# Optimization experiments

Hardware: AMD Instinct MI355X
Metric: run time of the kernel (lower is better)

Reference implementation:

```python
import jax, jax.numpy as jnp
import numpy as np

RO = 0.5      # backtracking shrink factor (default ro)
C = 1e-4      # Armijo constant (default c)


def setup_inputs() -> dict:
    B, TX = 65536, 8
    n = 2 * TX
    key = jax.random.key(0)
    k1, k2, k3 = jax.random.split(key, 3)
    y = jax.random.normal(k1, (B, n), dtype=jnp.float32)
    h = jax.random.normal(k2, (B, n, n), dtype=jnp.float32)
    bits = jax.random.randint(k3, (B, n, 1), 0, 2)
    x0 = (2 * bits - 1).astype(jnp.float32)  # random +/-1 init (torch.randint path)
    return {"y": y, "h": h, "x0": x0, "iteration": 10}


def reference(y, h, x0, iteration):
    B, n = y.shape
    y3 = y[..., None]                      # [B, n, 1]
    hT = jnp.swapaxes(h, 1, 2)             # [B, n, n]
    h_k = jnp.tile(jnp.eye(n, dtype=y.dtype)[None], (B, 1, 1))
    x = x0
    alpha = jnp.ones((B,), dtype=y.dtype)  # NOTE: alpha persists across outer iters, as in torch

    def f_val(xc):                         # torch.norm(y - h x, dim=1) / 2 -> [B, 1]
        r = y3 - h @ xc
        return 0.5 * jnp.sqrt(jnp.sum(r * r, axis=1))

    def g_val(xc):                         # H^T (H x - y) -> [B, n, 1]
        return hT @ (h @ xc - y3)

    for _ in range(iteration):
        g = g_val(x)
        p = -(h_k @ g)                     # search direction [B, n, 1]

        # --- backtracking line search (Armijo), batched; cond is any() over batch ---
        fx = f_val(x)[:, 0]                                    # [B]
        gtp = (jnp.swapaxes(g, 1, 2) @ p)[:, 0, 0]             # [B]

        def _lhs(a):
            return f_val(x + a[:, None, None] * p)[:, 0]

        def cond_fn(a):
            return jnp.any(_lhs(a) > fx + C * a * gtp)

        def body_fn(a):
            return jnp.where(_lhs(a) > fx + C * a * gtp, RO * a, a)

        alpha = jax.lax.while_loop(cond_fn, body_fn, alpha)

        # --- step + BFGS inverse-Hessian update (as written in the source) ---
        x_new = x + alpha[:, None, None] * p
        s = x_new - x                                          # [B, n, 1]
        yk = g_val(x_new) - g                                  # [B, n, 1]
        sT = jnp.swapaxes(s, 1, 2)
        ykT = jnp.swapaxes(yk, 1, 2)
        auxSc = sT @ yk                                        # [B, 1, 1]
        h_k = (h_k
               + (auxSc + ykT @ (h_k @ yk)) * (s @ sT) / auxSc ** 2
               - ((h_k @ (yk @ sT)) + s @ (ykT @ h_k)) / auxSc)
        x = x_new

    return x[..., 0]                       # [B, n]
```

## Files before the change

kernel.cpp:

```cpp
#include <hip/hip_runtime.h>


#define QN_N 16

__device__ __forceinline__ float redsum16(float v) {
    v += __shfl_xor(v, 1);
    v += __shfl_xor(v, 2);
    v += __shfl_xor(v, 4);
    v += __shfl_xor(v, 8);
    return v;
}

__device__ __forceinline__ float dot16(const float* a, const float* b) {
    float s0 = 0.f, s1 = 0.f, s2 = 0.f, s3 = 0.f;
#pragma unroll
    for (int k = 0; k < QN_N; k += 4) {
        s0 = fmaf(a[k + 0], b[k + 0], s0);
        s1 = fmaf(a[k + 1], b[k + 1], s1);
        s2 = fmaf(a[k + 2], b[k + 2], s2);
        s3 = fmaf(a[k + 3], b[k + 3], s3);
    }
    return (s0 + s1) + (s2 + s3);
}

#define BCAST(val, dst)                                   \
    do {                                                  \
        __builtin_amdgcn_wave_barrier();                  \
        slot[l] = (val);                                  \
        __builtin_amdgcn_wave_barrier();                  \
        float4 b0_ = ((const float4*)slot)[0];            \
        float4 b1_ = ((const float4*)slot)[1];            \
        float4 b2_ = ((const float4*)slot)[2];            \
        float4 b3_ = ((const float4*)slot)[3];            \
        (dst)[0] = b0_.x; (dst)[1] = b0_.y;               \
        (dst)[2] = b0_.z; (dst)[3] = b0_.w;               \
        (dst)[4] = b1_.x; (dst)[5] = b1_.y;               \
        (dst)[6] = b1_.z; (dst)[7] = b1_.w;               \
        (dst)[8] = b2_.x; (dst)[9] = b2_.y;               \
        (dst)[10] = b2_.z; (dst)[11] = b2_.w;             \
        (dst)[12] = b3_.x; (dst)[13] = b3_.y;             \
        (dst)[14] = b3_.z; (dst)[15] = b3_.w;             \
    } while (0)

__global__ __launch_bounds__(256, 4) void qn_kernel(
    const float* __restrict__ y, const float* __restrict__ h,
    const float* __restrict__ x0, const int* __restrict__ iter_p,
    float* __restrict__ out, int B)
{
    const int tid = blockIdx.x * blockDim.x + threadIdx.x;
    const int batch = tid >> 4;
    const int l = threadIdx.x & 15;
    if (batch >= B) return;
    const int iters = iter_p[0];

    __shared__ __align__(16) float bc[16][QN_N];
    float* slot = bc[threadIdx.x >> 4];

    const float* hb = h + (size_t)batch * (QN_N * QN_N);
    float hrow[QN_N], hcol[QN_N], hk[QN_N];
    {
        const float4* r4 = (const float4*)(hb + l * QN_N);
#pragma unroll
        for (int q = 0; q < 4; ++q) {
            float4 v = r4[q];
            hrow[4 * q + 0] = v.x; hrow[4 * q + 1] = v.y;
            hrow[4 * q + 2] = v.z; hrow[4 * q + 3] = v.w;
        }
    }
#pragma unroll
    for (int i = 0; i < QN_N; ++i) hcol[i] = hb[i * QN_N + l];
#pragma unroll
    for (int i = 0; i < QN_N; ++i) hk[i] = (i == l) ? 1.0f : 0.0f;

    const float yl = y[batch * QN_N + l];
    float xl = x0[batch * QN_N + l];
    float alpha = 1.0f;

    float tmp[QN_N];

    BCAST(xl, tmp);
    float hx = dot16(hrow, tmp);
    BCAST(hx - yl, tmp);
    float g = dot16(hcol, tmp);

    for (int it = 0; it < iters; ++it) {
        BCAST(g, tmp);
        float p = -dot16(hk, tmp);
        float gtp = redsum16(g * p);
        BCAST(p, tmp);
        float hp = dot16(hrow, tmp);
        float r0 = yl - hx;
        float fx = 0.5f * sqrtf(redsum16(r0 * r0));

        float a = alpha;
        float hxa;
        for (;;) {
            hxa = hx + a * hp;
            float res = yl - hxa;
            float lhs = 0.5f * sqrtf(redsum16(res * res));
            float rhs = fx + 1e-4f * a * gtp;
            bool fail = lhs > rhs;
            if (!__any(fail)) break;
            if (fail) a *= 0.5f;
        }
        alpha = a;

        float ap = a * p;
        float xn = xl + ap;
        float s = xn - xl;
        float hxn = hxa;

        BCAST(hxn - yl, tmp);
        float gn = dot16(hcol, tmp);
        float yk = gn - g;

        BCAST(yk, tmp);
        float hy = dot16(hk, tmp);

        float aux = redsum16(s * yk);
        float yhy = redsum16(yk * hy);
        float inv_aux = 1.0f / aux;
        float inv_aux2 = 1.0f / (aux * aux);
        float A1 = aux + yhy;

        float sv[QN_N], hyv[QN_N];
        BCAST(s, sv);
        BCAST(hy, hyv);
#pragma unroll
        for (int k = 0; k < QN_N; ++k) {
            float t1 = (A1 * (s * sv[k])) * inv_aux2;
            float t2 = (hy * sv[k] + s * hyv[k]) * inv_aux;
            hk[k] = (hk[k] + t1) - t2;
        }

        xl = xn;
        hx = hxn;
        g = gn;
    }

    out[batch * QN_N + l] = xl;
}

extern "C" void kernel_launch(void* const* d_in, const int* in_sizes, int n_in,
                              void* d_out, int out_size, void* d_ws, size_t ws_size,
                              hipStream_t stream) {
    const float* y  = (const float*)d_in[0];
    const float* h  = (const float*)d_in[1];
    const float* x0 = (const float*)d_in[2];
    const int* itp  = (const int*)d_in[3];
    float* out = (float*)d_out;

    const int B = in_sizes[0] / QN_N;
    const int threads = B * QN_N;
    const int blocks = (threads + 255) / 256;
    qn_kernel<<<blocks, 256, 0, stream>>>(y, h, x0, itp, out, B);
}
```

Before: 174.3 us.

## Use packed f32x2 FMAs, merge reductions and broadcasts, refactor BFGS update

Converts the per-lane 16-element dot products and the inverse-Hessian row update to two-wide float vectors so the compiler can emit packed FP32 FMA instructions. Pairs of independent 16-lane shuffle reductions and two shared-memory broadcasts are merged into single passes, and the shared slot is widened to hold both broadcast vectors. The BFGS update is refactored by precomputing the per-lane scalar coefficients, which changes floating-point rounding order slightly. The goal is fewer VALU instructions and fewer barrier/shuffle round trips per iteration.

```diff
diff --git a/kernel.cpp b/kernel.cpp
--- a/kernel.cpp
+++ b/kernel.cpp
@@ -2,6 +2,10 @@
 
 
 #define QN_N 16
+
+typedef float f32x2 __attribute__((ext_vector_type(2)));
+
+#define SLOT_STRIDE 40
 
 __device__ __forceinline__ float redsum16(float v) {
     v += __shfl_xor(v, 1);
@@ -11,35 +15,59 @@
     return v;
 }
 
-__device__ __forceinline__ float dot16(const float* a, const float* b) {
-    float s0 = 0.f, s1 = 0.f, s2 = 0.f, s3 = 0.f;
+__device__ __forceinline__ f32x2 redsum16p(f32x2 v) {
 #pragma unroll
-    for (int k = 0; k < QN_N; k += 4) {
-        s0 = fmaf(a[k + 0], b[k + 0], s0);
-        s1 = fmaf(a[k + 1], b[k + 1], s1);
-        s2 = fmaf(a[k + 2], b[k + 2], s2);
-        s3 = fmaf(a[k + 3], b[k + 3], s3);
+    for (int m = 1; m <= 8; m <<= 1) {
+        f32x2 o;
+        o.x = __shfl_xor(v.x, m);
+        o.y = __shfl_xor(v.y, m);
+        v = v + o;
     }
-    return (s0 + s1) + (s2 + s3);
+    return v;
 }
 
-#define BCAST(val, dst)                                   \
-    do {                                                  \
-        __builtin_amdgcn_wave_barrier();                  \
-        slot[l] = (val);                                  \
-        __builtin_amdgcn_wave_barrier();                  \
-        float4 b0_ = ((const float4*)slot)[0];            \
-        float4 b1_ = ((const float4*)slot)[1];            \
-        float4 b2_ = ((const float4*)slot)[2];            \
-        float4 b3_ = ((const float4*)slot)[3];            \
-        (dst)[0] = b0_.x; (dst)[1] = b0_.y;               \
-        (dst)[2] = b0_.z; (dst)[3] = b0_.w;               \
-        (dst)[4] = b1_.x; (dst)[5] = b1_.y;               \
-        (dst)[6] = b1_.z; (dst)[7] = b1_.w;               \
-        (dst)[8] = b2_.x; (dst)[9] = b2_.y;               \
-        (dst)[10] = b2_.z; (dst)[11] = b2_.w;             \
-        (dst)[12] = b3_.x; (dst)[13] = b3_.y;             \
-        (dst)[14] = b3_.z; (dst)[15] = b3_.w;             \
+__device__ __forceinline__ float dot16p(const f32x2* a, const f32x2* b) {
+    f32x2 s0 = {0.f, 0.f}, s1 = {0.f, 0.f}, s2 = {0.f, 0.f}, s3 = {0.f, 0.f};
+    s0 = __builtin_elementwise_fma(a[0], b[0], s0);
+    s1 = __builtin_elementwise_fma(a[1], b[1], s1);
+    s2 = __builtin_elementwise_fma(a[2], b[2], s2);
+    s3 = __builtin_elementwise_fma(a[3], b[3], s3);
+    s0 = __builtin_elementwise_fma(a[4], b[4], s0);
+    s1 = __builtin_elementwise_fma(a[5], b[5], s1);
+    s2 = __builtin_elementwise_fma(a[6], b[6], s2);
+    s3 = __builtin_elementwise_fma(a[7], b[7], s3);
+    f32x2 t = (s0 + s1) + (s2 + s3);
+    return t.x + t.y;
+}
+
+#define BCASTP(val, dst2)                                  \
+    do {                                                   \
+        __builtin_amdgcn_wave_barrier();                   \
+        slot[l] = (val);                                   \
+        __builtin_amdgcn_wave_barrier();                   \
+        _Pragma("unroll")                                  \
+        for (int q_ = 0; q_ < 4; ++q_) {                   \
+            float4 f_ = ((const float4*)slot)[q_];         \
+            (dst2)[2 * q_]     = (f32x2){f_.x, f_.y};      \
+            (dst2)[2 * q_ + 1] = (f32x2){f_.z, f_.w};      \
+        }                                                  \
+    } while (0)
+
+#define BCAST2P(va, vb, dstA2, dstB2)                      \
+    do {                                                   \
+        __builtin_amdgcn_wave_barrier();                   \
+        slot[l] = (va);                                    \
+        slot[16 + l] = (vb);                               \
+        __builtin_amdgcn_wave_barrier();                   \
+        _Pragma("unroll")                                  \
+        for (int q_ = 0; q_ < 4; ++q_) {                   \
+            float4 fa_ = ((const float4*)slot)[q_];        \
+            float4 fb_ = ((const float4*)(slot + 16))[q_]; \
+            (dstA2)[2 * q_]     = (f32x2){fa_.x, fa_.y};   \
+            (dstA2)[2 * q_ + 1] = (f32x2){fa_.z, fa_.w};   \
+            (dstB2)[2 * q_]     = (f32x2){fb_.x, fb_.y};   \
+            (dstB2)[2 * q_ + 1] = (f32x2){fb_.z, fb_.w};   \
+        }                                                  \
     } while (0)
 
 __global__ __launch_bounds__(256, 4) void qn_kernel(
@@ -53,44 +81,48 @@
     if (batch >= B) return;
     const int iters = iter_p[0];
 
-    __shared__ __align__(16) float bc[16][QN_N];
+    __shared__ __align__(16) float bc[16][SLOT_STRIDE];
     float* slot = bc[threadIdx.x >> 4];
 
     const float* hb = h + (size_t)batch * (QN_N * QN_N);
-    float hrow[QN_N], hcol[QN_N], hk[QN_N];
+    f32x2 hrow2[8], hcol2[8], hk2[8];
     {
         const float4* r4 = (const float4*)(hb + l * QN_N);
 #pragma unroll
         for (int q = 0; q < 4; ++q) {
             float4 v = r4[q];
-            hrow[4 * q + 0] = v.x; hrow[4 * q + 1] = v.y;
-            hrow[4 * q + 2] = v.z; hrow[4 * q + 3] = v.w;
+            hrow2[2 * q]     = (f32x2){v.x, v.y};
+            hrow2[2 * q + 1] = (f32x2){v.z, v.w};
         }
     }
 #pragma unroll
-    for (int i = 0; i < QN_N; ++i) hcol[i] = hb[i * QN_N + l];
+    for (int i = 0; i < 8; ++i)
+        hcol2[i] = (f32x2){hb[(2 * i) * QN_N + l], hb[(2 * i + 1) * QN_N + l]};
 #pragma unroll
-    for (int i = 0; i < QN_N; ++i) hk[i] = (i == l) ? 1.0f : 0.0f;
+    for (int i = 0; i < 8; ++i)
+        hk2[i] = (f32x2){(2 * i == l) ? 1.0f : 0.0f, (2 * i + 1 == l) ? 1.0f : 0.0f};
 
     const float yl = y[batch * QN_N + l];
     float xl = x0[batch * QN_N + l];
     float alpha = 1.0f;
 
-    float tmp[QN_N];
+    f32x2 tmp2[8];
 
-    BCAST(xl, tmp);
-    float hx = dot16(hrow, tmp);
-    BCAST(hx - yl, tmp);
-    float g = dot16(hcol, tmp);
+    BCASTP(xl, tmp2);
+    float hx = dot16p(hrow2, tmp2);
+    BCASTP(hx - yl, tmp2);
+    float g = dot16p(hcol2, tmp2);
 
     for (int it = 0; it < iters; ++it) {
-        BCAST(g, tmp);
-        float p = -dot16(hk, tmp);
-        float gtp = redsum16(g * p);
-        BCAST(p, tmp);
-        float hp = dot16(hrow, tmp);
+        BCASTP(g, tmp2);
+        float p = -dot16p(hk2, tmp2);
+        BCASTP(p, tmp2);
+        float hp = dot16p(hrow2, tmp2);
+
         float r0 = yl - hx;
-        float fx = 0.5f * sqrtf(redsum16(r0 * r0));
+        f32x2 pr = redsum16p((f32x2){g * p, r0 * r0});
+        float gtp = pr.x;
+        float fx = 0.5f * sqrtf(pr.y);
 
         float a = alpha;
         float hxa;
@@ -105,32 +137,35 @@
         }
         alpha = a;
 
-        float ap = a * p;
-        float xn = xl + ap;
+        float xn = xl + a * p;
         float s = xn - xl;
         float hxn = hxa;
 
-        BCAST(hxn - yl, tmp);
-        float gn = dot16(hcol, tmp);
+        BCASTP(hxn - yl, tmp2);
+        float gn = dot16p(hcol2, tmp2);
         float yk = gn - g;
 
-        BCAST(yk, tmp);
-        float hy = dot16(hk, tmp);
+        BCASTP(yk, tmp2);
+        float hy = dot16p(hk2, tmp2);
 
-        float aux = redsum16(s * yk);
-        float yhy = redsum16(yk * hy);
+        f32x2 ay = redsum16p((f32x2){s * yk, yk * hy});
+        float aux = ay.x, yhy = ay.y;
         float inv_aux = 1.0f / aux;
         float inv_aux2 = 1.0f / (aux * aux);
         float A1 = aux + yhy;
 
-        float sv[QN_N], hyv[QN_N];
-        BCAST(s, sv);
-        BCAST(hy, hyv);
+        f32x2 sv2[8], hyv2[8];
+        BCAST2P(s, hy, sv2, hyv2);
+        float c1s = (A1 * inv_aux2) * s;
+        float c2s = s * inv_aux;
+        float c3s = hy * inv_aux;
+        f32x2 c1p = {c1s, c1s}, c2p = {c2s, c2s}, c3p = {c3s, c3s};
 #pragma unroll
-        for (int k = 0; k < QN_N; ++k) {
-            float t1 = (A1 * (s * sv[k])) * inv_aux2;
-            float t2 = (hy * sv[k] + s * hyv[k]) * inv_aux;
-            hk[k] = (hk[k] + t1) - t2;
+        for (int j = 0; j < 8; ++j) {
+            f32x2 u = __builtin_elementwise_fma(c1p, sv2[j], hk2[j]);
+            f32x2 t = c3p * sv2[j];
+            t = __builtin_elementwise_fma(c2p, hyv2[j], t);
+            hk2[j] = u - t;
         }
 
         xl = xn;
```

After: 169.0 us. 1.03x faster.
